# Kernel optimization log

Measured on AMD Instinct MI355X. Metric: run time of the kernel, lower is better.

Reference implementation:

```python
import jax, jax.numpy as jnp
import numpy as np

N, E, IN, HID, HEADS, OUT = 50000, 800000, 128, 32, 4, 2
NEG = 0.2   # LeakyReLU negative slope (PyG default)
EPS = 1e-5  # BatchNorm eps


def setup_inputs() -> dict:
    key = jax.random.key(0)
    ks = jax.random.split(key, 32)
    g = lambda i, shape, s=0.05: (jax.random.normal(ks[i], shape, jnp.float32) * s)
    d = {
        'x': jax.random.normal(ks[0], (N, IN), jnp.float32),
        'edge_index': jax.random.randint(ks[1], (2, E), 0, N, jnp.int32),
        'edge_attr': jax.random.normal(ks[2], (E, 1), jnp.float32),
        # conv1: GATv2, in=IN, out=HID, heads=HEADS, edge_dim=1
        'c1_Wl': g(3, (IN, HEADS * HID)), 'c1_bl': g(4, (HEADS * HID,)),
        'c1_Wr': g(5, (IN, HEADS * HID)), 'c1_br': g(6, (HEADS * HID,)),
        'c1_We': g(7, (1, HEADS * HID)),
        'c1_att': g(8, (HEADS, HID)),
        'c1_bias': g(9, (HEADS * HID,)),
        'bn1_gamma': jnp.ones((HEADS * HID,), jnp.float32),
        'bn1_beta': jnp.zeros((HEADS * HID,), jnp.float32),
        'bn1_mean': g(10, (HEADS * HID,)),
        'bn1_var': jax.random.uniform(ks[11], (HEADS * HID,), jnp.float32, 0.5, 1.5),
        # conv2: GATv2, in=HEADS*HID, out=HID, heads=1, edge_dim=1
        'c2_Wl': g(12, (HEADS * HID, HID)), 'c2_bl': g(13, (HID,)),
        'c2_Wr': g(14, (HEADS * HID, HID)), 'c2_br': g(15, (HID,)),
        'c2_We': g(16, (1, HID)),
        'c2_att': g(17, (1, HID)),
        'c2_bias': g(18, (HID,)),
        'bn2_gamma': jnp.ones((HID,), jnp.float32),
        'bn2_beta': jnp.zeros((HID,), jnp.float32),
        'bn2_mean': g(19, (HID,)),
        'bn2_var': jax.random.uniform(ks[20], (HID,), jnp.float32, 0.5, 1.5),
        # classifier
        'clf_W': g(21, (HID, OUT)), 'clf_b': g(22, (OUT,)),
    }
    return d


def _gatv2(x, src, dst, eattr, Wl, bl, Wr, br, We, att, bias, heads, out_ch, concat):
    n = x.shape[0]
    xl = (x @ Wl + bl).reshape(n, heads, out_ch)   # source transform
    xr = (x @ Wr + br).reshape(n, heads, out_ch)   # target transform
    el = (eattr @ We).reshape(-1, heads, out_ch)   # edge transform (no bias in PyG)
    s = xl[src] + xr[dst] + el                     # [E, H, C]
    s = jnp.where(s > 0, s, NEG * s)               # LeakyReLU
    logits = jnp.einsum('ehc,hc->eh', s, att)      # [E, H]
    # segment softmax over destination nodes (every node has a self-loop)
    m = jax.ops.segment_max(logits, dst, num_segments=n)
    a = jnp.exp(logits - m[dst])
    denom = jax.ops.segment_sum(a, dst, num_segments=n)
    alpha = a / denom[dst]                         # [E, H]
    out = jax.ops.segment_sum(alpha[:, :, None] * xl[src], dst, num_segments=n)
    out = out.reshape(n, heads * out_ch) if concat else out.mean(axis=1)
    return out + bias


def _bn_eval(x, gamma, beta, mean, var):
    return (x - mean) * (gamma / jnp.sqrt(var + EPS)) + beta


def reference(x, edge_index, edge_attr,
              c1_Wl, c1_bl, c1_Wr, c1_br, c1_We, c1_att, c1_bias,
              bn1_gamma, bn1_beta, bn1_mean, bn1_var,
              c2_Wl, c2_bl, c2_Wr, c2_br, c2_We, c2_att, c2_bias,
              bn2_gamma, bn2_beta, bn2_mean, bn2_var,
              clf_W, clf_b):
    n = x.shape[0]
    # add self-loops once (PyG GATv2 default add_self_loops=True, fill_value='mean')
    loop = jnp.arange(n, dtype=edge_index.dtype)
    src = jnp.concatenate([edge_index[0], loop])
    dst = jnp.concatenate([edge_index[1], loop])
    loop_attr = jnp.broadcast_to(edge_attr.mean(axis=0, keepdims=True), (n, edge_attr.shape[1]))
    eattr = jnp.concatenate([edge_attr, loop_attr], axis=0)

    h = _gatv2(x, src, dst, eattr, c1_Wl, c1_bl, c1_Wr, c1_br, c1_We, c1_att, c1_bias,
               HEADS, HID, True)
    h = jax.nn.relu(_bn_eval(h, bn1_gamma, bn1_beta, bn1_mean, bn1_var))
    # dropout inactive in eval mode
    h = _gatv2(h, src, dst, eattr, c2_Wl, c2_bl, c2_Wr, c2_br, c2_We, c2_att, c2_bias,
               1, HID, True)
    h = jax.nn.relu(_bn_eval(h, bn2_gamma, bn2_beta, bn2_mean, bn2_var))
    return h @ clf_W + clf_b
```

## Files before the change

### kernel.cpp

```cpp
#include <hip/hip_runtime.h>

#define NNODES 50000
#define NEDGES 800000
#define ETOT   850000
#define IN_CH  128
#define HID    32
#define C1     128
#define NEG    0.2f
#define BNEPS  1e-5f
#define XFB2   1563
#define HB4    782
#define WTS    160
#define XSS    136
#define NC     16
#define SCB    196
#define FEB    782
#define FLB    49
#define EB1    2048
#define EB2    2048

typedef __attribute__((ext_vector_type(8))) short short8;
typedef __attribute__((ext_vector_type(4))) float f32x4;

__device__ __forceinline__ unsigned short bf16r(float f) {
    unsigned u = __float_as_uint(f);
    return (unsigned short)((u + 0x7fffu + ((u >> 16) & 1u)) >> 16);
}
__device__ __forceinline__ unsigned bf16pair(float f0, float f1) {
    return (unsigned)bf16r(f0) | ((unsigned)bf16r(f1) << 16);
}
__device__ __forceinline__ float blo(unsigned u) { return __uint_as_float(u << 16); }
__device__ __forceinline__ float bhi(unsigned u) { return __uint_as_float(u & 0xffff0000u); }

__device__ __forceinline__ int block_iscan(int v, int* ls) {
    int lane = threadIdx.x & 63, w = threadIdx.x >> 6;
    #pragma unroll
    for (int o = 1; o < 64; o <<= 1) {
        int t = __shfl_up(v, o);
        if (lane >= o) v += t;
    }
    if (lane == 63) ls[w] = v;
    __syncthreads();
    int add = 0;
    #pragma unroll
    for (int i = 0; i < 4; i++) add += (i < w) ? ls[i] : 0;
    return v + add;
}

__global__ __launch_bounds__(256) void k_prep(const float* __restrict__ Wl1,
                                              const float* __restrict__ Wr1,
                                              const float* __restrict__ Wl2,
                                              const float* __restrict__ Wr2,
                                              unsigned short* __restrict__ WT,
                                              unsigned short* __restrict__ WT2,
                                              int* __restrict__ hist,
                                              float* __restrict__ meanbuf) {
    int idx = blockIdx.x * 256 + threadIdx.x;
    if (idx == 0) meanbuf[0] = 0.f;
    for (int i = idx; i < NC * NNODES; i += 160 * 256) hist[i] = 0;
    if (idx < 32768) {
        int mat = idx >> 14, rem = idx & 16383;
        int k = rem >> 7, n = rem & 127;
        float v = mat ? Wr1[k * 128 + n] : Wl1[k * 128 + n];
        WT[(size_t)(mat * 128 + n) * WTS + k] = bf16r(v);
    } else {
        int i2 = idx - 32768;
        int mat = i2 >> 12, rem = i2 & 4095;
        int k = rem >> 5, n = rem & 31;
        float v = mat ? Wr2[k * 32 + n] : Wl2[k * 32 + n];
        WT2[(size_t)(mat * 32 + n) * WTS + k] = bf16r(v);
    }
}

__global__ __launch_bounds__(256) void k_xf_eh(
    const float* __restrict__ x,
    const float* __restrict__ bl, const float* __restrict__ br,
    const unsigned short* __restrict__ WT,
    unsigned* __restrict__ xlb, float* __restrict__ xr,
    const int* __restrict__ ei, const float* __restrict__ ea,
    int* __restrict__ hist, int* __restrict__ eoff,
    float* __restrict__ meanbuf) {
    __shared__ short xs_s[64 * XSS];
    int bi = blockIdx.x;
    if (bi % 3 == 0) {
        float* ls = (float*)xs_s;
        int hb = bi / 3;
        int e0 = hb * 1024 + threadIdx.x;
        float v = 0.f;
        if (hb < HB4 - 1) {
            #pragma unroll
            for (int j = 0; j < 4; j++) {
                int e = e0 + 256 * j;
                int c = (4 * hb + j) & (NC - 1);
                eoff[e] = atomicAdd(&hist[c * NNODES + ei[NEDGES + e]], 1);
                v += ea[e];
            }
        } else {
            #pragma unroll
            for (int j = 0; j < 4; j++) {
                int e = e0 + 256 * j;
                if (e < NEDGES) {
                    int c = (4 * hb + j) & (NC - 1);
                    eoff[e] = atomicAdd(&hist[c * NNODES + ei[NEDGES + e]], 1);
                    v += ea[e];
                }
            }
        }
        #pragma unroll
        for (int o = 32; o > 0; o >>= 1) v += __shfl_down(v, o, 64);
        if ((threadIdx.x & 63) == 0) ls[threadIdx.x >> 6] = v;
        __syncthreads();
        if (threadIdx.x == 0) atomicAdd(meanbuf, ls[0] + ls[1] + ls[2] + ls[3]);
        return;
    }
    int g = bi - bi / 3 - 1;
    if (g >= XFB2) return;
    int n0g = g * 32;
    {
        int nd = threadIdx.x >> 3, kc = (threadIdx.x & 7) * 16;
        bool valid = (n0g + nd) < NNODES;
        float xv[16];
        #pragma unroll
        for (int i = 0; i < 4; i++) {
            float4 t = valid ? ((const float4*)(x + (size_t)(n0g + nd) * IN_CH + kc))[i]
                             : make_float4(0.f, 0.f, 0.f, 0.f);
            xv[4 * i] = t.x; xv[4 * i + 1] = t.y; xv[4 * i + 2] = t.z; xv[4 * i + 3] = t.w;
        }
        unsigned hi[8], lo[8];
        #pragma unroll
        for (int i = 0; i < 8; i++) {
            unsigned short h0 = bf16r(xv[2 * i]), h1 = bf16r(xv[2 * i + 1]);
            float l0 = xv[2 * i]     - __uint_as_float(((unsigned)h0) << 16);
            float l1 = xv[2 * i + 1] - __uint_as_float(((unsigned)h1) << 16);
            hi[i] = (unsigned)h0 | ((unsigned)h1 << 16);
            lo[i] = bf16pair(l0, l1);
        }
        uint4* ph = (uint4*)&xs_s[nd * XSS + kc];
        ph[0] = make_uint4(hi[0], hi[1], hi[2], hi[3]);
        ph[1] = make_uint4(hi[4], hi[5], hi[6], hi[7]);
        uint4* pl = (uint4*)&xs_s[(nd + 32) * XSS + kc];
        pl[0] = make_uint4(lo[0], lo[1], lo[2], lo[3]);
        pl[1] = make_uint4(lo[4], lo[5], lo[6], lo[7]);
    }
    __syncthreads();
    int lane = threadIdx.x & 63;
    int lm = lane & 15, q = lane >> 4;
    int w = threadIdx.x >> 6;
    int n0 = w * 64;
    f32x4 acc[2][4];
    #pragma unroll
    for (int mt = 0; mt < 2; mt++)
        #pragma unroll
        for (int nt = 0; nt < 4; nt++) acc[mt][nt] = (f32x4)0.f;

    #pragma unroll
    for (int ks = 0; ks < 4; ks++) {
        int k0 = ks * 32 + q * 8;
        short8 ah0 = *(const short8*)&xs_s[(lm)      * XSS + k0];
        short8 ah1 = *(const short8*)&xs_s[(16 + lm) * XSS + k0];
        short8 al0 = *(const short8*)&xs_s[(32 + lm) * XSS + k0];
        short8 al1 = *(const short8*)&xs_s[(48 + lm) * XSS + k0];
        #pragma unroll
        for (int nt = 0; nt < 4; nt++) {
            short8 bfr = *(const short8*)(WT + (size_t)(n0 + nt * 16 + lm) * WTS + k0);
            acc[0][nt] = __builtin_amdgcn_mfma_f32_16x16x32_bf16(al0, bfr, acc[0][nt], 0, 0, 0);
            acc[0][nt] = __builtin_amdgcn_mfma_f32_16x16x32_bf16(ah0, bfr, acc[0][nt], 0, 0, 0);
            acc[1][nt] = __builtin_amdgcn_mfma_f32_16x16x32_bf16(al1, bfr, acc[1][nt], 0, 0, 0);
            acc[1][nt] = __builtin_amdgcn_mfma_f32_16x16x32_bf16(ah1, bfr, acc[1][nt], 0, 0, 0);
        }
    }
    if (w < 2) {
        #pragma unroll
        for (int nt = 0; nt < 4; nt++) {
            int ch = n0 + nt * 16 + lm;
            float bv = bl[ch];
            #pragma unroll
            for (int mt = 0; mt < 2; mt++)
                #pragma unroll
                for (int r = 0; r < 4; r++) {
                    int node = n0g + mt * 16 + q * 4 + r;
                    float val = acc[mt][nt][r] + bv;
                    float pv = __shfl_xor(val, 1);
                    if ((lm & 1) == 0 && node < NNODES)
                        xlb[(size_t)node * 64 + (ch >> 1)] = bf16pair(val, pv);
                }
        }
    } else {
        #pragma unroll
        for (int nt = 0; nt < 4; nt++) {
            int ch = n0 - 128 + nt * 16 + lm;
            float bv = br[ch];
            #pragma unroll
            for (int mt = 0; mt < 2; mt++)
                #pragma unroll
                for (int r = 0; r < 4; r++) {
                    int node = n0g + mt * 16 + q * 4 + r;
                    if (node < NNODES)
                        xr[(size_t)node * C1 + ch] = acc[mt][nt][r] + bv;
                }
        }
    }
}

__global__ __launch_bounds__(256) void k_red(int* __restrict__ hist,
                                             int* __restrict__ deg,
                                             int* __restrict__ bsum) {
    __shared__ int ls[4];
    int d = blockIdx.x * 256 + threadIdx.x;
    int s = 0;
    if (d < NNODES) {
        #pragma unroll
        for (int c = 0; c < NC; c++) {
            int v = hist[c * NNODES + d];
            hist[c * NNODES + d] = s;
            s += v;
        }
        deg[d] = s;
    }
    int v = (d < NNODES) ? s + 1 : 0;
    #pragma unroll
    for (int o = 32; o > 0; o >>= 1) v += __shfl_down(v, o, 64);
    if ((threadIdx.x & 63) == 0) ls[threadIdx.x >> 6] = v;
    __syncthreads();
    if (threadIdx.x == 0) bsum[blockIdx.x] = ls[0] + ls[1] + ls[2] + ls[3];
}

__global__ __launch_bounds__(256) void k_rowp(const int* __restrict__ deg,
                                              const int* __restrict__ bsum,
                                              int* __restrict__ rowptr) {
    __shared__ int ls[4];
    int t = threadIdx.x;
    int bv = (t < SCB) ? bsum[t] : 0;
    int bincl = block_iscan(bv, ls);
    __shared__ int boffs[256];
    boffs[t] = bincl - bv;
    __syncthreads();
    int base = boffs[blockIdx.x];
    __syncthreads();
    int d = blockIdx.x * 256 + t;
    int v = (d < NNODES) ? deg[d] + 1 : 0;
    int incl = block_iscan(v, ls);
    if (d < NNODES) rowptr[d] = base + incl - v;
    if (d == NNODES - 1) rowptr[NNODES] = base + incl;
}

__global__ __launch_bounds__(256) void k_fill(const int* __restrict__ ei,
                                              const float* __restrict__ ea,
                                              const int* __restrict__ rowptr,
                                              const float* __restrict__ meanbuf,
                                              const int* __restrict__ hist,
                                              const int* __restrict__ eoff,
                                              unsigned* __restrict__ cpack) {
    int blk = blockIdx.x, tid = threadIdx.x;
    if (blk < FEB) {
        int e0 = blk * 1024 + tid;
        int d[4], sv[4], rp[4], hs[4], eo[4];
        float av[4];
        bool ok[4];
        #pragma unroll
        for (int j = 0; j < 4; j++) {
            int e = e0 + 256 * j;
            ok[j] = e < NEDGES;
            int es = ok[j] ? e : 0;
            d[j]  = ei[NEDGES + es];
            sv[j] = ei[es];
            av[j] = ea[es];
            eo[j] = eoff[es];
        }
        #pragma unroll
        for (int j = 0; j < 4; j++) {
            int e = e0 + 256 * j;
            int c = (e >> 8) & (NC - 1);
            rp[j] = rowptr[d[j]];
            hs[j] = hist[c * NNODES + d[j]];
        }
        #pragma unroll
        for (int j = 0; j < 4; j++)
            if (ok[j])
                cpack[rp[j] + 1 + hs[j] + eo[j]] =
                    ((unsigned)bf16r(av[j]) << 16) | (unsigned)sv[j];
        return;
    }
    if (blk < FEB + FLB) {
        float mv = meanbuf[0] * (1.0f / NEDGES);
        unsigned mp = ((unsigned)bf16r(mv)) << 16;
        int i0 = (blk - FEB) * 1024 + tid;
        int rp[4];
        bool ok[4];
        #pragma unroll
        for (int j = 0; j < 4; j++) {
            int i = i0 + 256 * j;
            ok[j] = i < NNODES;
            rp[j] = rowptr[ok[j] ? i : 0];
        }
        #pragma unroll
        for (int j = 0; j < 4; j++)
            if (ok[j]) cpack[rp[j]] = mp | (unsigned)(i0 + 256 * j);
        return;
    }
    if (tid < 64) cpack[ETOT + tid] = 0u;
}

__global__ __launch_bounds__(256) void k_edge1(
    const unsigned* __restrict__ xlb, const float* __restrict__ xr,
    const int* __restrict__ rowptr, const unsigned* __restrict__ cpack,
    const float* __restrict__ We, const float* __restrict__ att,
    float* __restrict__ out1) {
    int lane = threadIdx.x & 63;
    int q = lane & 15, s = lane >> 4;
    int node = blockIdx.x * 4 + (threadIdx.x >> 6);
    if (node >= NNODES) return;
    const int W = EB1 * 4;
    float4 we0 = ((const float4*)We)[2 * q],  we1 = ((const float4*)We)[2 * q + 1];
    float4 at0 = ((const float4*)att)[2 * q], at1 = ((const float4*)att)[2 * q + 1];
    const uint4* xlv = (const uint4*)xlb;
    int r0 = rowptr[node], r1 = rowptr[node + 1];
    float4 xr0 = ((const float4*)xr)[(size_t)node * 32 + 2 * q];
    float4 xr1 = ((const float4*)xr)[(size_t)node * 32 + 2 * q + 1];
    for (;;) {
        int nn = node + W;
        bool more = nn < NNODES;
        int nr0 = 0, nr1 = 0;
        float4 nxr0 = make_float4(0.f, 0.f, 0.f, 0.f);
        float4 nxr1 = make_float4(0.f, 0.f, 0.f, 0.f);
        if (more) {
            nr0 = rowptr[nn]; nr1 = rowptr[nn + 1];
            nxr0 = ((const float4*)xr)[(size_t)nn * 32 + 2 * q];
            nxr1 = ((const float4*)xr)[(size_t)nn * 32 + 2 * q + 1];
        }
        float den = 0.f;
        float a0 = 0.f, a1 = 0.f, a2 = 0.f, a3 = 0.f;
        float a4 = 0.f, a5 = 0.f, a6 = 0.f, a7 = 0.f;
        int nit = (r1 - r0 + 3) >> 2;
        int k = r0 + s;
        unsigned sc0 = cpack[k];
        uint4 xv0 = xlv[(size_t)(sc0 & 0xffffu) * 16 + q];
        unsigned sc1 = cpack[k + 4];
        uint4 xv1 = xlv[(size_t)(sc1 & 0xffffu) * 16 + q];
        for (int it = 0; it < nit; it++) {
            unsigned scn = cpack[k + 8];
            uint4 xvn = xlv[(size_t)(scn & 0xffffu) * 16 + q];
            bool ok = k < r1;
            float av = __uint_as_float(sc0 & 0xffff0000u);
            float x0 = blo(xv0.x), x1 = bhi(xv0.x), x2 = blo(xv0.y), x3 = bhi(xv0.y);
            float x4 = blo(xv0.z), x5 = bhi(xv0.z), x6 = blo(xv0.w), x7 = bhi(xv0.w);
            float v0 = x0 + xr0.x + av * we0.x;  v0 = v0 > 0.f ? v0 : NEG * v0;
            float v1 = x1 + xr0.y + av * we0.y;  v1 = v1 > 0.f ? v1 : NEG * v1;
            float v2 = x2 + xr0.z + av * we0.z;  v2 = v2 > 0.f ? v2 : NEG * v2;
            float v3 = x3 + xr0.w + av * we0.w;  v3 = v3 > 0.f ? v3 : NEG * v3;
            float v4 = x4 + xr1.x + av * we1.x;  v4 = v4 > 0.f ? v4 : NEG * v4;
            float v5 = x5 + xr1.y + av * we1.y;  v5 = v5 > 0.f ? v5 : NEG * v5;
            float v6 = x6 + xr1.z + av * we1.z;  v6 = v6 > 0.f ? v6 : NEG * v6;
            float v7 = x7 + xr1.w + av * we1.w;  v7 = v7 > 0.f ? v7 : NEG * v7;
            float t = v0 * at0.x + v1 * at0.y + v2 * at0.z + v3 * at0.w
                    + v4 * at1.x + v5 * at1.y + v6 * at1.z + v7 * at1.w;
            t += __shfl_xor(t, 1);
            t += __shfl_xor(t, 2);
            float e = ok ? __expf(t) : 0.f;
            den += e;
            a0 = fmaf(e, x0, a0); a1 = fmaf(e, x1, a1);
            a2 = fmaf(e, x2, a2); a3 = fmaf(e, x3, a3);
            a4 = fmaf(e, x4, a4); a5 = fmaf(e, x5, a5);
            a6 = fmaf(e, x6, a6); a7 = fmaf(e, x7, a7);
            k += 4;
            sc0 = sc1; xv0 = xv1;
            sc1 = scn; xv1 = xvn;
        }
        #pragma unroll
        for (int o = 16; o <= 32; o <<= 1) {
            den += __shfl_xor(den, o);
            a0 += __shfl_xor(a0, o); a1 += __shfl_xor(a1, o);
            a2 += __shfl_xor(a2, o); a3 += __shfl_xor(a3, o);
            a4 += __shfl_xor(a4, o); a5 += __shfl_xor(a5, o);
            a6 += __shfl_xor(a6, o); a7 += __shfl_xor(a7, o);
        }
        if (s == 0) {
            float rd = 1.f / den;
            ((float4*)out1)[(size_t)node * 32 + 2 * q] =
                make_float4(a0 * rd, a1 * rd, a2 * rd, a3 * rd);
            ((float4*)out1)[(size_t)node * 32 + 2 * q + 1] =
                make_float4(a4 * rd, a5 * rd, a6 * rd, a7 * rd);
        }
        if (!more) return;
        node = nn; r0 = nr0; r1 = nr1; xr0 = nxr0; xr1 = nxr1;
    }
}

__global__ __launch_bounds__(256) void k_epi(
    const float* __restrict__ out1, const float* __restrict__ bias1,
    const float* __restrict__ g1, const float* __restrict__ b1,
    const float* __restrict__ m1, const float* __restrict__ v1,
    const unsigned short* __restrict__ WT2,
    const float* __restrict__ bl2, const float* __restrict__ br2,
    unsigned* __restrict__ xlb2, float* __restrict__ xr2) {
    __shared__ short hs_s[64 * XSS];
    __shared__ float A[128], B[128];
    int n0g = blockIdx.x * 32;
    if (threadIdx.x < 128) {
        int c = threadIdx.x;
        float sc = g1[c] * rsqrtf(v1[c] + BNEPS);
        A[c] = sc;
        B[c] = (bias1[c] - m1[c]) * sc + b1[c];
    }
    __syncthreads();
    {
        int nd = threadIdx.x >> 3, kc = (threadIdx.x & 7) * 16;
        bool valid = (n0g + nd) < NNODES;
        float xv[16];
        #pragma unroll
        for (int i = 0; i < 4; i++) {
            float4 t = valid ? ((const float4*)(out1 + (size_t)(n0g + nd) * C1 + kc))[i]
                             : make_float4(0.f, 0.f, 0.f, 0.f);
            xv[4 * i] = t.x; xv[4 * i + 1] = t.y; xv[4 * i + 2] = t.z; xv[4 * i + 3] = t.w;
        }
        #pragma unroll
        for (int j = 0; j < 16; j++)
            xv[j] = fmaxf(xv[j] * A[kc + j] + B[kc + j], 0.f);
        unsigned hi[8], lo[8];
        #pragma unroll
        for (int i = 0; i < 8; i++) {
            unsigned short h0 = bf16r(xv[2 * i]), h1 = bf16r(xv[2 * i + 1]);
            float l0 = xv[2 * i]     - __uint_as_float(((unsigned)h0) << 16);
            float l1 = xv[2 * i + 1] - __uint_as_float(((unsigned)h1) << 16);
            hi[i] = (unsigned)h0 | ((unsigned)h1 << 16);
            lo[i] = bf16pair(l0, l1);
        }
        uint4* ph = (uint4*)&hs_s[nd * XSS + kc];
        ph[0] = make_uint4(hi[0], hi[1], hi[2], hi[3]);
        ph[1] = make_uint4(hi[4], hi[5], hi[6], hi[7]);
        uint4* pl = (uint4*)&hs_s[(nd + 32) * XSS + kc];
        pl[0] = make_uint4(lo[0], lo[1], lo[2], lo[3]);
        pl[1] = make_uint4(lo[4], lo[5], lo[6], lo[7]);
    }
    __syncthreads();
    int lane = threadIdx.x & 63;
    int lm = lane & 15, q = lane >> 4;
    int w = threadIdx.x >> 6;
    f32x4 acc[2];
    acc[0] = (f32x4)0.f; acc[1] = (f32x4)0.f;
    #pragma unroll
    for (int ks = 0; ks < 4; ks++) {
        int k0 = ks * 32 + q * 8;
        short8 ah0 = *(const short8*)&hs_s[(lm)      * XSS + k0];
        short8 ah1 = *(const short8*)&hs_s[(16 + lm) * XSS + k0];
        short8 al0 = *(const short8*)&hs_s[(32 + lm) * XSS + k0];
        short8 al1 = *(const short8*)&hs_s[(48 + lm) * XSS + k0];
        short8 bfr = *(const short8*)(WT2 + (size_t)(w * 16 + lm) * WTS + k0);
        acc[0] = __builtin_amdgcn_mfma_f32_16x16x32_bf16(al0, bfr, acc[0], 0, 0, 0);
        acc[0] = __builtin_amdgcn_mfma_f32_16x16x32_bf16(ah0, bfr, acc[0], 0, 0, 0);
        acc[1] = __builtin_amdgcn_mfma_f32_16x16x32_bf16(al1, bfr, acc[1], 0, 0, 0);
        acc[1] = __builtin_amdgcn_mfma_f32_16x16x32_bf16(ah1, bfr, acc[1], 0, 0, 0);
    }
    if (w < 2) {
        int ch = w * 16 + lm;
        float bv = bl2[ch];
        #pragma unroll
        for (int mt = 0; mt < 2; mt++)
            #pragma unroll
            for (int r = 0; r < 4; r++) {
                int node = n0g + mt * 16 + q * 4 + r;
                float val = acc[mt][r] + bv;
                float pv = __shfl_xor(val, 1);
                if ((lm & 1) == 0 && node < NNODES)
                    xlb2[(size_t)node * 16 + (ch >> 1)] = bf16pair(val, pv);
            }
    } else {
        int ch = (w - 2) * 16 + lm;
        float bv = br2[ch];
        #pragma unroll
        for (int mt = 0; mt < 2; mt++)
            #pragma unroll
            for (int r = 0; r < 4; r++) {
                int node = n0g + mt * 16 + q * 4 + r;
                if (node < NNODES)
                    xr2[(size_t)node * HID + ch] = acc[mt][r] + bv;
            }
    }
}

__global__ __launch_bounds__(256) void k_edge2(
    const unsigned* __restrict__ xlb2, const float* __restrict__ xr2,
    const int* __restrict__ rowptr, const unsigned* __restrict__ cpack,
    const float* __restrict__ We2, const float* __restrict__ att2,
    const float* __restrict__ bias2,
    const float* __restrict__ g2, const float* __restrict__ b2,
    const float* __restrict__ m2, const float* __restrict__ v2,
    const float* __restrict__ W, const float* __restrict__ b,
    float* __restrict__ y) {
    int lane = threadIdx.x & 63;
    int q = lane & 3, s = lane >> 2;
    int node = blockIdx.x * 4 + (threadIdx.x >> 6);
    if (node >= NNODES) return;
    const int WV = EB2 * 4;
    float4 we0 = ((const float4*)We2)[2 * q],  we1 = ((const float4*)We2)[2 * q + 1];
    float4 at0 = ((const float4*)att2)[2 * q], at1 = ((const float4*)att2)[2 * q + 1];
    float4 gv0 = ((const float4*)g2)[2 * q],    gv1 = ((const float4*)g2)[2 * q + 1];
    float4 bv0 = ((const float4*)b2)[2 * q],    bv1 = ((const float4*)b2)[2 * q + 1];
    float4 mv0 = ((const float4*)m2)[2 * q],    mv1 = ((const float4*)m2)[2 * q + 1];
    float4 vv0 = ((const float4*)v2)[2 * q],    vv1 = ((const float4*)v2)[2 * q + 1];
    float4 bi0 = ((const float4*)bias2)[2 * q], bi1 = ((const float4*)bias2)[2 * q + 1];
    float4 sA0, sA1, sB0, sB1;
    sA0.x = gv0.x * rsqrtf(vv0.x + BNEPS); sB0.x = (bi0.x - mv0.x) * sA0.x + bv0.x;
    sA0.y = gv0.y * rsqrtf(vv0.y + BNEPS); sB0.y = (bi0.y - mv0.y) * sA0.y + bv0.y;
    sA0.z = gv0.z * rsqrtf(vv0.z + BNEPS); sB0.z = (bi0.z - mv0.z) * sA0.z + bv0.z;
    sA0.w = gv0.w * rsqrtf(vv0.w + BNEPS); sB0.w = (bi0.w - mv0.w) * sA0.w + bv0.w;
    sA1.x = gv1.x * rsqrtf(vv1.x + BNEPS); sB1.x = (bi1.x - mv1.x) * sA1.x + bv1.x;
    sA1.y = gv1.y * rsqrtf(vv1.y + BNEPS); sB1.y = (bi1.y - mv1.y) * sA1.y + bv1.y;
    sA1.z = gv1.z * rsqrtf(vv1.z + BNEPS); sB1.z = (bi1.z - mv1.z) * sA1.z + bv1.z;
    sA1.w = gv1.w * rsqrtf(vv1.w + BNEPS); sB1.w = (bi1.w - mv1.w) * sA1.w + bv1.w;
    float4 w0 = ((const float4*)W)[4 * q];
    float4 w1 = ((const float4*)W)[4 * q + 1];
    float4 w2 = ((const float4*)W)[4 * q + 2];
    float4 w3 = ((const float4*)W)[4 * q + 3];
    float bb0 = b[0], bb1 = b[1];
    const uint4* xlv = (const uint4*)xlb2;
    int r0 = rowptr[node], r1 = rowptr[node + 1];
    float4 xr0 = ((const float4*)xr2)[(size_t)node * 8 + 2 * q];
    float4 xr1 = ((const float4*)xr2)[(size_t)node * 8 + 2 * q + 1];
    for (;;) {
        int nn = node + WV;
        bool more = nn < NNODES;
        int nr0 = 0, nr1 = 0;
        float4 nxr0 = make_float4(0.f, 0.f, 0.f, 0.f);
        float4 nxr1 = make_float4(0.f, 0.f, 0.f, 0.f);
        if (more) {
            nr0 = rowptr[nn]; nr1 = rowptr[nn + 1];
            nxr0 = ((const float4*)xr2)[(size_t)nn * 8 + 2 * q];
            nxr1 = ((const float4*)xr2)[(size_t)nn * 8 + 2 * q + 1];
        }
        float den = 0.f;
        float a0 = 0.f, a1 = 0.f, a2 = 0.f, a3 = 0.f;
        float a4 = 0.f, a5 = 0.f, a6 = 0.f, a7 = 0.f;
        int nit = (r1 - r0 + 15) >> 4;
        int k = r0 + s;
        unsigned sc = cpack[k];
        uint4 xv = xlv[(size_t)(sc & 0xffffu) * 4 + q];
        for (int it = 0; it < nit; it++) {
            unsigned scn = cpack[k + 16];
            uint4 xvn = xlv[(size_t)(scn & 0xffffu) * 4 + q];
            bool ok = k < r1;
            float av = __uint_as_float(sc & 0xffff0000u);
            float x0 = blo(xv.x), x1 = bhi(xv.x), x2 = blo(xv.y), x3 = bhi(xv.y);
            float x4 = blo(xv.z), x5 = bhi(xv.z), x6 = blo(xv.w), x7 = bhi(xv.w);
            float v0 = x0 + xr0.x + av * we0.x;  v0 = v0 > 0.f ? v0 : NEG * v0;
            float v1 = x1 + xr0.y + av * we0.y;  v1 = v1 > 0.f ? v1 : NEG * v1;
            float v2 = x2 + xr0.z + av * we0.z;  v2 = v2 > 0.f ? v2 : NEG * v2;
            float v3 = x3 + xr0.w + av * we0.w;  v3 = v3 > 0.f ? v3 : NEG * v3;
            float v4 = x4 + xr1.x + av * we1.x;  v4 = v4 > 0.f ? v4 : NEG * v4;
            float v5 = x5 + xr1.y + av * we1.y;  v5 = v5 > 0.f ? v5 : NEG * v5;
            float v6 = x6 + xr1.z + av * we1.z;  v6 = v6 > 0.f ? v6 : NEG * v6;
            float v7 = x7 + xr1.w + av * we1.w;  v7 = v7 > 0.f ? v7 : NEG * v7;
            float t = v0 * at0.x + v1 * at0.y + v2 * at0.z + v3 * at0.w
                    + v4 * at1.x + v5 * at1.y + v6 * at1.z + v7 * at1.w;
            t += __shfl_xor(t, 1);
            t += __shfl_xor(t, 2);
            float e = ok ? __expf(t) : 0.f;
            den += e;
            a0 = fmaf(e, x0, a0); a1 = fmaf(e, x1, a1);
            a2 = fmaf(e, x2, a2); a3 = fmaf(e, x3, a3);
            a4 = fmaf(e, x4, a4); a5 = fmaf(e, x5, a5);
            a6 = fmaf(e, x6, a6); a7 = fmaf(e, x7, a7);
            k += 16; sc = scn; xv = xvn;
        }
        #pragma unroll
        for (int o = 4; o <= 32; o <<= 1) {
            den += __shfl_xor(den, o);
            a0 += __shfl_xor(a0, o); a1 += __shfl_xor(a1, o);
            a2 += __shfl_xor(a2, o); a3 += __shfl_xor(a3, o);
            a4 += __shfl_xor(a4, o); a5 += __shfl_xor(a5, o);
            a6 += __shfl_xor(a6, o); a7 += __shfl_xor(a7, o);
        }
        float rd = 1.f / den;
        float h0 = fmaxf(fmaf(a0 * rd, sA0.x, sB0.x), 0.f);
        float h1 = fmaxf(fmaf(a1 * rd, sA0.y, sB0.y), 0.f);
        float h2 = fmaxf(fmaf(a2 * rd, sA0.z, sB0.z), 0.f);
        float h3 = fmaxf(fmaf(a3 * rd, sA0.w, sB0.w), 0.f);
        float h4 = fmaxf(fmaf(a4 * rd, sA1.x, sB1.x), 0.f);
        float h5 = fmaxf(fmaf(a5 * rd, sA1.y, sB1.y), 0.f);
        float h6 = fmaxf(fmaf(a6 * rd, sA1.z, sB1.z), 0.f);
        float h7 = fmaxf(fmaf(a7 * rd, sA1.w, sB1.w), 0.f);
        float t0 = h0 * w0.x + h1 * w0.z + h2 * w1.x + h3 * w1.z
                 + h4 * w2.x + h5 * w2.z + h6 * w3.x + h7 * w3.z;
        float t1 = h0 * w0.y + h1 * w0.w + h2 * w1.y + h3 * w1.w
                 + h4 * w2.y + h5 * w2.w + h6 * w3.y + h7 * w3.w;
        t0 += __shfl_xor(t0, 1); t0 += __shfl_xor(t0, 2);
        t1 += __shfl_xor(t1, 1); t1 += __shfl_xor(t1, 2);
        if (lane == 0) {
            y[(size_t)node * 2]     = t0 + bb0;
            y[(size_t)node * 2 + 1] = t1 + bb1;
        }
        if (!more) return;
        node = nn; r0 = nr0; r1 = nr1; xr0 = nxr0; xr1 = nxr1;
    }
}

extern "C" void kernel_launch(void* const* d_in, const int* in_sizes, int n_in,
                              void* d_out, int out_size, void* d_ws, size_t ws_size,
                              hipStream_t stream) {
    const float* x       = (const float*)d_in[0];
    const int*   ei      = (const int*)d_in[1];
    const float* ea      = (const float*)d_in[2];
    const float* c1_Wl   = (const float*)d_in[3];
    const float* c1_bl   = (const float*)d_in[4];
    const float* c1_Wr   = (const float*)d_in[5];
    const float* c1_br   = (const float*)d_in[6];
    const float* c1_We   = (const float*)d_in[7];
    const float* c1_att  = (const float*)d_in[8];
    const float* c1_bias = (const float*)d_in[9];
    const float* bn1_g   = (const float*)d_in[10];
    const float* bn1_b   = (const float*)d_in[11];
    const float* bn1_m   = (const float*)d_in[12];
    const float* bn1_v   = (const float*)d_in[13];
    const float* c2_Wl   = (const float*)d_in[14];
    const float* c2_bl   = (const float*)d_in[15];
    const float* c2_Wr   = (const float*)d_in[16];
    const float* c2_br   = (const float*)d_in[17];
    const float* c2_We   = (const float*)d_in[18];
    const float* c2_att  = (const float*)d_in[19];
    const float* c2_bias = (const float*)d_in[20];
    const float* bn2_g   = (const float*)d_in[21];
    const float* bn2_b   = (const float*)d_in[22];
    const float* bn2_m   = (const float*)d_in[23];
    const float* bn2_v   = (const float*)d_in[24];
    const float* clf_W   = (const float*)d_in[25];
    const float* clf_b   = (const float*)d_in[26];

    float* ws = (float*)d_ws;
    size_t off = 0;
    unsigned* XLb  = (unsigned*)(ws + off); off += (size_t)NNODES * 64;
    float*    XR1  = ws + off; off += (size_t)NNODES * C1;
    float*    OUT1 = ws + off; off += (size_t)NNODES * C1;
    unsigned* XLb2 = (unsigned*)(ws + off); off += (size_t)NNODES * 16;
    float*    XR2  = ws + off; off += (size_t)NNODES * HID;
    unsigned* CPACK= (unsigned*)(ws + off); off += (size_t)ETOT + 64;
    unsigned short* WT  = (unsigned short*)(ws + off); off += 256 * WTS / 2;
    unsigned short* WT2 = (unsigned short*)(ws + off); off += 64 * WTS / 2;
    int*      EOFF = (int*)(ws + off); off += NEDGES;
    int*      ROWP = (int*)(ws + off); off += NNODES + 16;
    int*      DEG  = (int*)(ws + off); off += NNODES;
    int*      BSUM = (int*)(ws + off); off += 256;
    int*      HIST = (int*)(ws + off); off += (size_t)NC * NNODES;
    float*    MEANB= ws + off; off += 64;
    if (ws_size < off * sizeof(float)) return;

    k_prep  <<<160, 256, 0, stream>>>(c1_Wl, c1_Wr, c2_Wl, c2_Wr, WT, WT2, HIST, MEANB);
    k_xf_eh <<<3 * HB4, 256, 0, stream>>>(x, c1_bl, c1_br, WT, XLb, XR1,
                                          ei, ea, HIST, EOFF, MEANB);
    k_red   <<<SCB, 256, 0, stream>>>(HIST, DEG, BSUM);
    k_rowp  <<<SCB, 256, 0, stream>>>(DEG, BSUM, ROWP);
    k_fill  <<<FEB + FLB + 1, 256, 0, stream>>>(ei, ea, ROWP, MEANB, HIST, EOFF, CPACK);
    k_edge1 <<<EB1, 256, 0, stream>>>(XLb, XR1, ROWP, CPACK, c1_We, c1_att, OUT1);
    k_epi   <<<XFB2, 256, 0, stream>>>(OUT1, c1_bias, bn1_g, bn1_b, bn1_m, bn1_v,
                                       WT2, c2_bl, c2_br, XLb2, XR2);
    k_edge2 <<<EB2, 256, 0, stream>>>(XLb2, XR2, ROWP, CPACK, c2_We, c2_att,
                                      c2_bias, bn2_g, bn2_b, bn2_m, bn2_v,
                                      clf_W, clf_b, (float*)d_out);
}
```

Before: 294.2 us.

## Fold LeakyReLU into abs form with exp2, deepen edge prefetch, rebalance edge2 lanes

The LeakyReLU in both attention kernels becomes 0.6*s + 0.4*|s|, with log2(e) folded into the attention weights so `__expf` can be replaced by a native exp2. The edge1 gather pipeline goes from two to three in-flight neighbour loads. The edge2 kernel is reorganised so 8 lanes handle each edge's 32 channels and 8 edges are processed in parallel per wavefront, also with a three-deep prefetch. The histogram part of the fused transform/histogram kernel now handles 8 edges per thread, which changes the grid interleave ratio. The aim is fewer ALU ops per edge and better memory-latency hiding, at the cost of more registers per thread.

```diff
diff --git a/kernel.cpp b/kernel.cpp
--- a/kernel.cpp
+++ b/kernel.cpp
@@ -9,7 +9,8 @@
 #define NEG    0.2f
 #define BNEPS  1e-5f
 #define XFB2   1563
-#define HB4    782
+#define HB8    391
+#define XFEB   1955
 #define WTS    160
 #define XSS    136
 #define NC     16
@@ -18,6 +19,16 @@
 #define FLB    49
 #define EB1    2048
 #define EB2    2048
+#define L2E    1.4426950408889634f
+
+#if defined(__has_builtin)
+#if __has_builtin(__builtin_amdgcn_exp2f)
+#define EXP2F(x) __builtin_amdgcn_exp2f(x)
+#endif
+#endif
+#ifndef EXP2F
+#define EXP2F(x) exp2f(x)
+#endif
 
 typedef __attribute__((ext_vector_type(8))) short short8;
 typedef __attribute__((ext_vector_type(4))) float f32x4;
@@ -82,25 +93,25 @@
     float* __restrict__ meanbuf) {
     __shared__ short xs_s[64 * XSS];
     int bi = blockIdx.x;
-    if (bi % 3 == 0) {
+    if (bi % 5 == 0) {
         float* ls = (float*)xs_s;
-        int hb = bi / 3;
-        int e0 = hb * 1024 + threadIdx.x;
+        int hb = bi / 5;
+        int e0 = hb * 2048 + threadIdx.x;
         float v = 0.f;
-        if (hb < HB4 - 1) {
+        if (hb < HB8 - 1) {
             #pragma unroll
-            for (int j = 0; j < 4; j++) {
+            for (int j = 0; j < 8; j++) {
                 int e = e0 + 256 * j;
-                int c = (4 * hb + j) & (NC - 1);
+                int c = (8 * hb + j) & (NC - 1);
                 eoff[e] = atomicAdd(&hist[c * NNODES + ei[NEDGES + e]], 1);
                 v += ea[e];
             }
         } else {
             #pragma unroll
-            for (int j = 0; j < 4; j++) {
+            for (int j = 0; j < 8; j++) {
                 int e = e0 + 256 * j;
                 if (e < NEDGES) {
-                    int c = (4 * hb + j) & (NC - 1);
+                    int c = (8 * hb + j) & (NC - 1);
                     eoff[e] = atomicAdd(&hist[c * NNODES + ei[NEDGES + e]], 1);
                     v += ea[e];
                 }
@@ -113,7 +124,7 @@
         if (threadIdx.x == 0) atomicAdd(meanbuf, ls[0] + ls[1] + ls[2] + ls[3]);
         return;
     }
-    int g = bi - bi / 3 - 1;
+    int g = bi - bi / 5 - 1;
     if (g >= XFB2) return;
     int n0g = g * 32;
     {
@@ -311,8 +322,13 @@
     int node = blockIdx.x * 4 + (threadIdx.x >> 6);
     if (node >= NNODES) return;
     const int W = EB1 * 4;
+    const float C6 = 0.6f * L2E, C4 = 0.4f * L2E;
     float4 we0 = ((const float4*)We)[2 * q],  we1 = ((const float4*)We)[2 * q + 1];
-    float4 at0 = ((const float4*)att)[2 * q], at1 = ((const float4*)att)[2 * q + 1];
+    float4 av0 = ((const float4*)att)[2 * q], av1 = ((const float4*)att)[2 * q + 1];
+    float4 aA0 = make_float4(av0.x * C6, av0.y * C6, av0.z * C6, av0.w * C6);
+    float4 aB0 = make_float4(av0.x * C4, av0.y * C4, av0.z * C4, av0.w * C4);
+    float4 aA1 = make_float4(av1.x * C6, av1.y * C6, av1.z * C6, av1.w * C6);
+    float4 aB1 = make_float4(av1.x * C4, av1.y * C4, av1.z * C4, av1.w * C4);
     const uint4* xlv = (const uint4*)xlb;
     int r0 = rowptr[node], r1 = rowptr[node + 1];
     float4 xr0 = ((const float4*)xr)[(size_t)node * 32 + 2 * q];
@@ -337,26 +353,35 @@
         uint4 xv0 = xlv[(size_t)(sc0 & 0xffffu) * 16 + q];
         unsigned sc1 = cpack[k + 4];
         uint4 xv1 = xlv[(size_t)(sc1 & 0xffffu) * 16 + q];
+        unsigned sc2 = cpack[k + 8];
+        uint4 xv2 = xlv[(size_t)(sc2 & 0xffffu) * 16 + q];
         for (int it = 0; it < nit; it++) {
-            unsigned scn = cpack[k + 8];
+            unsigned scn = cpack[k + 12];
             uint4 xvn = xlv[(size_t)(scn & 0xffffu) * 16 + q];
             bool ok = k < r1;
             float av = __uint_as_float(sc0 & 0xffff0000u);
             float x0 = blo(xv0.x), x1 = bhi(xv0.x), x2 = blo(xv0.y), x3 = bhi(xv0.y);
             float x4 = blo(xv0.z), x5 = bhi(xv0.z), x6 = blo(xv0.w), x7 = bhi(xv0.w);
-            float v0 = x0 + xr0.x + av * we0.x;  v0 = v0 > 0.f ? v0 : NEG * v0;
-            float v1 = x1 + xr0.y + av * we0.y;  v1 = v1 > 0.f ? v1 : NEG * v1;
-            float v2 = x2 + xr0.z + av * we0.z;  v2 = v2 > 0.f ? v2 : NEG * v2;
-            float v3 = x3 + xr0.w + av * we0.w;  v3 = v3 > 0.f ? v3 : NEG * v3;
-            float v4 = x4 + xr1.x + av * we1.x;  v4 = v4 > 0.f ? v4 : NEG * v4;
-            float v5 = x5 + xr1.y + av * we1.y;  v5 = v5 > 0.f ? v5 : NEG * v5;
-            float v6 = x6 + xr1.z + av * we1.z;  v6 = v6 > 0.f ? v6 : NEG * v6;
-            float v7 = x7 + xr1.w + av * we1.w;  v7 = v7 > 0.f ? v7 : NEG * v7;
-            float t = v0 * at0.x + v1 * at0.y + v2 * at0.z + v3 * at0.w
-                    + v4 * at1.x + v5 * at1.y + v6 * at1.z + v7 * at1.w;
+            float s0 = fmaf(av, we0.x, x0 + xr0.x);
+            float s1 = fmaf(av, we0.y, x1 + xr0.y);
+            float s2 = fmaf(av, we0.z, x2 + xr0.z);
+            float s3 = fmaf(av, we0.w, x3 + xr0.w);
+            float s4 = fmaf(av, we1.x, x4 + xr1.x);
+            float s5 = fmaf(av, we1.y, x5 + xr1.y);
+            float s6 = fmaf(av, we1.z, x6 + xr1.z);
+            float s7 = fmaf(av, we1.w, x7 + xr1.w);
+            float tA = s0 * aA0.x;            tA = fmaf(fabsf(s0), aB0.x, tA);
+            tA = fmaf(s1, aA0.y, tA);         tA = fmaf(fabsf(s1), aB0.y, tA);
+            tA = fmaf(s2, aA0.z, tA);         tA = fmaf(fabsf(s2), aB0.z, tA);
+            tA = fmaf(s3, aA0.w, tA);         tA = fmaf(fabsf(s3), aB0.w, tA);
+            float tB = s4 * aA1.x;            tB = fmaf(fabsf(s4), aB1.x, tB);
+            tB = fmaf(s5, aA1.y, tB);         tB = fmaf(fabsf(s5), aB1.y, tB);
+            tB = fmaf(s6, aA1.z, tB);         tB = fmaf(fabsf(s6), aB1.z, tB);
+            tB = fmaf(s7, aA1.w, tB);         tB = fmaf(fabsf(s7), aB1.w, tB);
+            float t = tA + tB;
             t += __shfl_xor(t, 1);
             t += __shfl_xor(t, 2);
-            float e = ok ? __expf(t) : 0.f;
+            float e = ok ? EXP2F(t) : 0.f;
             den += e;
             a0 = fmaf(e, x0, a0); a1 = fmaf(e, x1, a1);
             a2 = fmaf(e, x2, a2); a3 = fmaf(e, x3, a3);
@@ -364,7 +389,8 @@
             a6 = fmaf(e, x6, a6); a7 = fmaf(e, x7, a7);
             k += 4;
             sc0 = sc1; xv0 = xv1;
-            sc1 = scn; xv1 = xvn;
+            sc1 = sc2; xv1 = xv2;
+            sc2 = scn; xv2 = xvn;
         }
         #pragma unroll
         for (int o = 16; o <= 32; o <<= 1) {
@@ -488,109 +514,98 @@
     const float* __restrict__ W, const float* __restrict__ b,
     float* __restrict__ y) {
     int lane = threadIdx.x & 63;
-    int q = lane & 3, s = lane >> 2;
+    int q = lane & 7, s = lane >> 3;
     int node = blockIdx.x * 4 + (threadIdx.x >> 6);
     if (node >= NNODES) return;
     const int WV = EB2 * 4;
-    float4 we0 = ((const float4*)We2)[2 * q],  we1 = ((const float4*)We2)[2 * q + 1];
-    float4 at0 = ((const float4*)att2)[2 * q], at1 = ((const float4*)att2)[2 * q + 1];
-    float4 gv0 = ((const float4*)g2)[2 * q],    gv1 = ((const float4*)g2)[2 * q + 1];
-    float4 bv0 = ((const float4*)b2)[2 * q],    bv1 = ((const float4*)b2)[2 * q + 1];
-    float4 mv0 = ((const float4*)m2)[2 * q],    mv1 = ((const float4*)m2)[2 * q + 1];
-    float4 vv0 = ((const float4*)v2)[2 * q],    vv1 = ((const float4*)v2)[2 * q + 1];
-    float4 bi0 = ((const float4*)bias2)[2 * q], bi1 = ((const float4*)bias2)[2 * q + 1];
-    float4 sA0, sA1, sB0, sB1;
-    sA0.x = gv0.x * rsqrtf(vv0.x + BNEPS); sB0.x = (bi0.x - mv0.x) * sA0.x + bv0.x;
-    sA0.y = gv0.y * rsqrtf(vv0.y + BNEPS); sB0.y = (bi0.y - mv0.y) * sA0.y + bv0.y;
-    sA0.z = gv0.z * rsqrtf(vv0.z + BNEPS); sB0.z = (bi0.z - mv0.z) * sA0.z + bv0.z;
-    sA0.w = gv0.w * rsqrtf(vv0.w + BNEPS); sB0.w = (bi0.w - mv0.w) * sA0.w + bv0.w;
-    sA1.x = gv1.x * rsqrtf(vv1.x + BNEPS); sB1.x = (bi1.x - mv1.x) * sA1.x + bv1.x;
-    sA1.y = gv1.y * rsqrtf(vv1.y + BNEPS); sB1.y = (bi1.y - mv1.y) * sA1.y + bv1.y;
-    sA1.z = gv1.z * rsqrtf(vv1.z + BNEPS); sB1.z = (bi1.z - mv1.z) * sA1.z + bv1.z;
-    sA1.w = gv1.w * rsqrtf(vv1.w + BNEPS); sB1.w = (bi1.w - mv1.w) * sA1.w + bv1.w;
-    float4 w0 = ((const float4*)W)[4 * q];
-    float4 w1 = ((const float4*)W)[4 * q + 1];
-    float4 w2 = ((const float4*)W)[4 * q + 2];
-    float4 w3 = ((const float4*)W)[4 * q + 3];
+    const float C6 = 0.6f * L2E, C4 = 0.4f * L2E;
+    float4 we = ((const float4*)We2)[q];
+    float4 av4 = ((const float4*)att2)[q];
+    float4 aA = make_float4(av4.x * C6, av4.y * C6, av4.z * C6, av4.w * C6);
+    float4 aB = make_float4(av4.x * C4, av4.y * C4, av4.z * C4, av4.w * C4);
+    float4 gv = ((const float4*)g2)[q];
+    float4 bv = ((const float4*)b2)[q];
+    float4 mv = ((const float4*)m2)[q];
+    float4 vv = ((const float4*)v2)[q];
+    float4 bi = ((const float4*)bias2)[q];
+    float4 sA, sB;
+    sA.x = gv.x * rsqrtf(vv.x + BNEPS); sB.x = (bi.x - mv.x) * sA.x + bv.x;
+    sA.y = gv.y * rsqrtf(vv.y + BNEPS); sB.y = (bi.y - mv.y) * sA.y + bv.y;
+    sA.z = gv.z * rsqrtf(vv.z + BNEPS); sB.z = (bi.z - mv.z) * sA.z + bv.z;
+    sA.w = gv.w * rsqrtf(vv.w + BNEPS); sB.w = (bi.w - mv.w) * sA.w + bv.w;
+    float4 w0 = ((const float4*)W)[2 * q];
+    float4 w1 = ((const float4*)W)[2 * q + 1];
     float bb0 = b[0], bb1 = b[1];
-    const uint4* xlv = (const uint4*)xlb2;
+    const uint2* xlv = (const uint2*)xlb2;
     int r0 = rowptr[node], r1 = rowptr[node + 1];
-    float4 xr0 = ((const float4*)xr2)[(size_t)node * 8 + 2 * q];
-    float4 xr1 = ((const float4*)xr2)[(size_t)node * 8 + 2 * q + 1];
+    float4 xr0 = ((const float4*)xr2)[(size_t)node * 8 + q];
     for (;;) {
         int nn = node + WV;
         bool more = nn < NNODES;
         int nr0 = 0, nr1 = 0;
         float4 nxr0 = make_float4(0.f, 0.f, 0.f, 0.f);
-        float4 nxr1 = make_float4(0.f, 0.f, 0.f, 0.f);
         if (more) {
             nr0 = rowptr[nn]; nr1 = rowptr[nn + 1];
-            nxr0 = ((const float4*)xr2)[(size_t)nn * 8 + 2 * q];
-            nxr1 = ((const float4*)xr2)[(size_t)nn * 8 + 2 * q + 1];
+            nxr0 = ((const float4*)xr2)[(size_t)nn * 8 + q];
         }
         float den = 0.f;
         float a0 = 0.f, a1 = 0.f, a2 = 0.f, a3 = 0.f;
-        float a4 = 0.f, a5 = 0.f, a6 = 0.f, a7 = 0.f;
-        int nit = (r1 - r0 + 15) >> 4;
+        int nit = (r1 - r0 + 7) >> 3;
         int k = r0 + s;
-        unsigned sc = cpack[k];
-        uint4 xv = xlv[(size_t)(sc & 0xffffu) * 4 + q];
+        unsigned sc0 = cpack[k];
+        uint2 xv0 = xlv[(size_t)(sc0 & 0xffffu) * 8 + q];
+        unsigned sc1 = cpack[k + 8];
+        uint2 xv1 = xlv[(size_t)(sc1 & 0xffffu) * 8 + q];
+        unsigned sc2 = cpack[k + 16];
+        uint2 xv2 = xlv[(size_t)(sc2 & 0xffffu) * 8 + q];
         for (int it = 0; it < nit; it++) {
-            unsigned scn = cpack[k + 16];
-            uint4 xvn = xlv[(size_t)(scn & 0xffffu) * 4 + q];
+            unsigned scn = cpack[k + 24];
+            uint2 xvn = xlv[(size_t)(scn & 0xffffu) * 8 + q];
             bool ok = k < r1;
-            float av = __uint_as_float(sc & 0xffff0000u);
-            float x0 = blo(xv.x), x1 = bhi(xv.x), x2 = blo(xv.y), x3 = bhi(xv.y);
-            float x4 = blo(xv.z), x5 = bhi(xv.z), x6 = blo(xv.w), x7 = bhi(xv.w);
-            float v0 = x0 + xr0.x + av * we0.x;  v0 = v0 > 0.f ? v0 : NEG * v0;
-            float v1 = x1 + xr0.y + av * we0.y;  v1 = v1 > 0.f ? v1 : NEG * v1;
-            float v2 = x2 + xr0.z + av * we0.z;  v2 = v2 > 0.f ? v2 : NEG * v2;
-            float v3 = x3 + xr0.w + av * we0.w;  v3 = v3 > 0.f ? v3 : NEG * v3;
-            float v4 = x4 + xr1.x + av * we1.x;  v4 = v4 > 0.f ? v4 : NEG * v4;
-            float v5 = x5 + xr1.y + av * we1.y;  v5 = v5 > 0.f ? v5 : NEG * v5;
-            float v6 = x6 + xr1.z + av * we1.z;  v6 = v6 > 0.f ? v6 : NEG * v6;
-            float v7 = x7 + xr1.w + av * we1.w;  v7 = v7 > 0.f ? v7 : NEG * v7;
-            float t = v0 * at0.x + v1 * at0.y + v2 * at0.z + v3 * at0.w
-                    + v4 * at1.x + v5 * at1.y + v6 * at1.z + v7 * at1.w;
+            float av = __uint_as_float(sc0 & 0xffff0000u);
+            float x0 = blo(xv0.x), x1 = bhi(xv0.x), x2 = blo(xv0.y), x3 = bhi(xv0.y);
+            float s0 = fmaf(av, we.x, x0 + xr0.x);
+            float s1 = fmaf(av, we.y, x1 + xr0.y);
+            float s2 = fmaf(av, we.z, x2 + xr0.z);
+            float s3 = fmaf(av, we.w, x3 + xr0.w);
+            float tA = s0 * aA.x;             tA = fmaf(fabsf(s0), aB.x, tA);
+            tA = fmaf(s1, aA.y, tA);          tA = fmaf(fabsf(s1), aB.y, tA);
+            float tB = s2 * aA.z;             tB = fmaf(fabsf(s2), aB.z, tB);
+            tB = fmaf(s3, aA.w, tB);          tB = fmaf(fabsf(s3), aB.w, tB);
+            float t = tA + tB;
             t += __shfl_xor(t, 1);
             t += __shfl_xor(t, 2);
-            float e = ok ? __expf(t) : 0.f;
+            t += __shfl_xor(t, 4);
+            float e = ok ? EXP2F(t) : 0.f;
             den += e;
             a0 = fmaf(e, x0, a0); a1 = fmaf(e, x1, a1);
             a2 = fmaf(e, x2, a2); a3 = fmaf(e, x3, a3);
-            a4 = fmaf(e, x4, a4); a5 = fmaf(e, x5, a5);
-            a6 = fmaf(e, x6, a6); a7 = fmaf(e, x7, a7);
-            k += 16; sc = scn; xv = xvn;
-        }
-        #pragma unroll
-        for (int o = 4; o <= 32; o <<= 1) {
+            k += 8;
+            sc0 = sc1; xv0 = xv1;
+            sc1 = sc2; xv1 = xv2;
+            sc2 = scn; xv2 = xvn;
+        }
+        #pragma unroll
+        for (int o = 8; o <= 32; o <<= 1) {
             den += __shfl_xor(den, o);
             a0 += __shfl_xor(a0, o); a1 += __shfl_xor(a1, o);
             a2 += __shfl_xor(a2, o); a3 += __shfl_xor(a3, o);
-            a4 += __shfl_xor(a4, o); a5 += __shfl_xor(a5, o);
-            a6 += __shfl_xor(a6, o); a7 += __shfl_xor(a7, o);
         }
         float rd = 1.f / den;
-        float h0 = fmaxf(fmaf(a0 * rd, sA0.x, sB0.x), 0.f);
-        float h1 = fmaxf(fmaf(a1 * rd, sA0.y, sB0.y), 0.f);
-        float h2 = fmaxf(fmaf(a2 * rd, sA0.z, sB0.z), 0.f);
-        float h3 = fmaxf(fmaf(a3 * rd, sA0.w, sB0.w), 0.f);
-        float h4 = fmaxf(fmaf(a4 * rd, sA1.x, sB1.x), 0.f);
-        float h5 = fmaxf(fmaf(a5 * rd, sA1.y, sB1.y), 0.f);
-        float h6 = fmaxf(fmaf(a6 * rd, sA1.z, sB1.z), 0.f);
-        float h7 = fmaxf(fmaf(a7 * rd, sA1.w, sB1.w), 0.f);
-        float t0 = h0 * w0.x + h1 * w0.z + h2 * w1.x + h3 * w1.z
-                 + h4 * w2.x + h5 * w2.z + h6 * w3.x + h7 * w3.z;
-        float t1 = h0 * w0.y + h1 * w0.w + h2 * w1.y + h3 * w1.w
-                 + h4 * w2.y + h5 * w2.w + h6 * w3.y + h7 * w3.w;
-        t0 += __shfl_xor(t0, 1); t0 += __shfl_xor(t0, 2);
-        t1 += __shfl_xor(t1, 1); t1 += __shfl_xor(t1, 2);
+        float h0 = fmaxf(fmaf(a0 * rd, sA.x, sB.x), 0.f);
+        float h1 = fmaxf(fmaf(a1 * rd, sA.y, sB.y), 0.f);
+        float h2 = fmaxf(fmaf(a2 * rd, sA.z, sB.z), 0.f);
+        float h3 = fmaxf(fmaf(a3 * rd, sA.w, sB.w), 0.f);
+        float u0 = h0 * w0.x + h1 * w0.z + h2 * w1.x + h3 * w1.z;
+        float u1 = h0 * w0.y + h1 * w0.w + h2 * w1.y + h3 * w1.w;
+        u0 += __shfl_xor(u0, 1); u0 += __shfl_xor(u0, 2); u0 += __shfl_xor(u0, 4);
+        u1 += __shfl_xor(u1, 1); u1 += __shfl_xor(u1, 2); u1 += __shfl_xor(u1, 4);
         if (lane == 0) {
-            y[(size_t)node * 2]     = t0 + bb0;
-            y[(size_t)node * 2 + 1] = t1 + bb1;
+            y[(size_t)node * 2]     = u0 + bb0;
+            y[(size_t)node * 2 + 1] = u1 + bb1;
         }
         if (!more) return;
-        node = nn; r0 = nr0; r1 = nr1; xr0 = nxr0; xr1 = nxr1;
+        node = nn; r0 = nr0; r1 = nr1; xr0 = nxr0;
     }
 }
 
@@ -644,8 +659,8 @@
     if (ws_size < off * sizeof(float)) return;
 
     k_prep  <<<160, 256, 0, stream>>>(c1_Wl, c1_Wr, c2_Wl, c2_Wr, WT, WT2, HIST, MEANB);
-    k_xf_eh <<<3 * HB4, 256, 0, stream>>>(x, c1_bl, c1_br, WT, XLb, XR1,
-                                          ei, ea, HIST, EOFF, MEANB);
+    k_xf_eh <<<XFEB, 256, 0, stream>>>(x, c1_bl, c1_br, WT, XLb, XR1,
+                                       ei, ea, HIST, EOFF, MEANB);
     k_red   <<<SCB, 256, 0, stream>>>(HIST, DEG, BSUM);
     k_rowp  <<<SCB, 256, 0, stream>>>(DEG, BSUM, ROWP);
     k_fill  <<<FEB + FLB + 1, 256, 0, stream>>>(ei, ea, ROWP, MEANB, HIST, EOFF, CPACK);
```

After: 294.5 us. No clear change (+0.1%).
